# Performance work log

Measured on AMD Instinct MI355X. Metric: run time of the kernel, lower is better.

The kernel has to match this reference:

```python
import jax, jax.numpy as jnp
import numpy as np

B, T, NV, DEG, E = 64, 256, 20000, 8, 128
NSEG, NBUCKET = NV * DEG, 288
F_DIST, F_DIR, F_TT, HID = 50, 50, 50, 100
FEED = 2 * E + F_DIST + F_DIR  # 356


def setup_inputs() -> dict:
    key = jax.random.key(0)
    ks = jax.random.split(key, 32)
    s = 1.0 / np.sqrt(E)
    return {
        "xs_padded": jax.random.randint(ks[0], (B, T), 0, NV),
        "lengths": jax.random.randint(ks[1], (B,), 8, T + 1),
        "xs_actions": jax.random.randint(ks[2], (B, T - 1), 0, DEG),
        "destinations": jax.random.randint(ks[3], (B,), 0, NV),
        "adj_list": jax.random.randint(ks[4], (NV, DEG), 0, NV),
        "seg_ids": jax.random.randint(ks[5], (NV, DEG), 0, NSEG),
        "start_time": 42,
        "locations": jax.random.normal(ks[6], (NV, 2)),
        "time_dist_seg": jax.random.uniform(ks[7], (NSEG, NBUCKET)) * 10.0,
        "emb": jax.random.normal(ks[8], (NV + 2, E)) * 0.01,
        "Wq": jax.random.normal(ks[9], (E, E)) * s,
        "Wk": jax.random.normal(ks[10], (E, E)) * s,
        "Wv": jax.random.normal(ks[11], (E, E)) * s,
        "Wo": jax.random.normal(ks[12], (E, E)) * s,
        "dist_W": jax.random.normal(ks[13], (1, F_DIST)),
        "dist_b": jnp.zeros((F_DIST,)),
        "dir_W": jax.random.normal(ks[14], (2, F_DIR)) * 0.7,
        "dir_b": jnp.zeros((F_DIR,)),
        "tt_W": jax.random.normal(ks[15], (1, F_TT)),
        "tt_b": jnp.zeros((F_TT,)),
        "ob_W1": jax.random.normal(ks[16], (F_TT, F_TT // 2)) * (1.0 / np.sqrt(F_TT)),
        "ob_b1": jnp.zeros((F_TT // 2,)),
        "ob_W2": jax.random.normal(ks[17], (F_TT // 2, 1)) * (1.0 / np.sqrt(F_TT // 2)),
        "ob_b2": jnp.zeros((1,)),
        "om_W1": jax.random.normal(ks[18], (FEED, HID)) * (1.0 / np.sqrt(FEED)),
        "om_b1": jnp.zeros((HID,)),
        "om_W2": jax.random.normal(ks[19], (HID, HID // 2)) * (1.0 / np.sqrt(HID)),
        "om_b2": jnp.zeros((HID // 2,)),
        "om_W3": jax.random.normal(ks[20], (HID // 2, 1)) * (1.0 / np.sqrt(HID // 2)),
        "om_b3": jnp.zeros((1,)),
    }


def reference(xs_padded, lengths, xs_actions, destinations, adj_list, seg_ids,
              start_time, locations, time_dist_seg, emb, Wq, Wk, Wv, Wo,
              dist_W, dist_b, dir_W, dir_b, tt_W, tt_b,
              ob_W1, ob_b1, ob_W2, ob_b2,
              om_W1, om_b1, om_W2, om_b2, om_W3, om_b3):
    # --- embeddings + causal/padding-masked self-attention (flash_att) ---
    x_e = emb[xs_padded]                                       # [B,T,E]
    q, k, v = x_e @ Wq, x_e @ Wk, x_e @ Wv
    scores = jnp.einsum('bqe,bke->bqk', q, k) / jnp.sqrt(jnp.float32(E))
    causal = jnp.triu(jnp.ones((T, T), bool), 1)
    pad = jnp.arange(T)[None, :] >= lengths[:, None]           # key padding [B,T]
    scores = jnp.where(causal[None] | pad[:, None, :], -1e9, scores)
    hidden = jnp.einsum('bqk,bke->bqe', jax.nn.softmax(scores, axis=-1), v) @ Wo

    # --- irregular neighbor gather: route_neighbors only filled for t < len-1 ---
    valid_t = jnp.arange(T)[None, :] < (lengths - 1)[:, None]  # [B,T]
    rn = jnp.where(valid_t[:, :, None], adj_list[xs_padded], 0)  # [B,T,DEG]

    # --- distance to destination feature ---
    dest_c = locations[destinations][:, None, None, :]         # [B,1,1,2]
    nbr_c = locations[rn]                                      # [B,T,DEG,2]
    dist = jnp.abs(nbr_c - dest_c).sum(-1, keepdims=True) * 100.0
    dist_f = dist @ dist_W + dist_b

    # --- direction (unit vector) feature ---
    vec = nbr_c - locations[xs_padded][:, :, None, :]
    unit = vec / (jnp.linalg.norm(vec, axis=-1, keepdims=True) + 1e-8)
    dir_f = unit @ dir_W + dir_b

    # --- travel-time lookup + masked whitening ---
    nmask = rn != 0
    tt = time_dist_seg[seg_ids[xs_padded], start_time]         # [B,T,DEG]
    mf = nmask.astype(tt.dtype)
    cnt = mf.sum()
    mean = (tt * mf).sum() / cnt
    var = (((tt - mean) ** 2) * mf).sum() / (cnt - 1.0)        # unbiased, like torch.std
    tt = (tt - mean) / (jnp.sqrt(var) + 1e-6)
    tt_f = (tt[..., None] @ tt_W + tt_b) * mf[..., None]

    # --- fuse and score neighbors ---
    hid_e = jnp.broadcast_to(hidden[:, :, None, :], (B, T, DEG, E))
    dest_e = jnp.broadcast_to(emb[destinations][:, None, None, :], (B, T, DEG, E))
    feed = jnp.concatenate([hid_e, dist_f, dir_f, dest_e], axis=-1)  # [B,T,DEG,356]

    ob = (jax.nn.relu(tt_f @ ob_W1 + ob_b1) @ ob_W2 + ob_b2).squeeze(-1)
    h1 = jax.nn.relu(feed @ om_W1 + om_b1)
    h2 = jax.nn.relu(h1 @ om_W2 + om_b2)
    logits = (h2 @ om_W3 + om_b3).squeeze(-1) + ob             # [B,T,DEG]

    # --- per-route mean cross-entropy over valid transitions, summed over batch ---
    logp = jax.nn.log_softmax(logits[:, :T - 1], axis=-1)
    nll = -jnp.take_along_axis(logp, xs_actions[..., None], axis=-1).squeeze(-1)
    vmask = (jnp.arange(T - 1)[None, :] < (lengths - 1)[:, None]).astype(nll.dtype)
    per = (nll * vmask).sum(1) / (lengths - 1).astype(nll.dtype)
    return per.sum()
```

## Files before the change

kernel.cpp:

```cpp
#include <hip/hip_runtime.h>
#include <math.h>

#define BB 64
#define TT 256
#define DEG 8
#define EE 128
#define NBUCKET 288
#define HID 100
#define H2 50

constexpr size_t OFF_STATS   = 0;
constexpr size_t OFF_CDIST   = 4;
constexpr size_t OFF_CDIRX   = 104;
constexpr size_t OFF_CDIRY   = 204;
constexpr size_t OFF_BASE    = 304;
constexpr size_t OFF_V25     = 404;
constexpr size_t OFF_C25     = 429;
constexpr size_t OFF_OBZ     = 454;
constexpr size_t OFF_DESTPRE = 456;
constexpr size_t OFF_WF      = 6856;
constexpr size_t OFF_W2P     = 19656;
constexpr size_t OFF_TT      = 32456;
constexpr size_t OFF_Q       = 163528;
constexpr size_t OFF_K       = OFF_Q + 16384 * 128;
constexpr size_t OFF_VP      = OFF_K + 16384 * 128;

__global__ void __launch_bounds__(256) k_setup(
    const int* destinations, const float* emb, const float* Wo,
    const float* dist_W, const float* dist_b, const float* dir_W, const float* dir_b,
    const float* tt_W, const float* tt_b, const float* ob_W1, const float* ob_b1,
    const float* ob_W2, const float* ob_b2, const float* om_W1, const float* om_b1,
    const float* om_W2, float* ws, float* out) {
    __shared__ float sh[EE];
    int blk = blockIdx.x;
    int j = threadIdx.x;
    if (blk == 0) {
        if (j < 4) ws[OFF_STATS + j] = 0.f;
        if (j == 0) out[0] = 0.f;
        if (j < HID) {
            float cd = 0.f, cx = 0.f, cy = 0.f, bs = om_b1[j];
            for (int f = 0; f < 50; f++) {
                float w1d = om_W1[(128 + f) * HID + j];
                float w1r = om_W1[(178 + f) * HID + j];
                cd += dist_W[f] * w1d;
                bs += dist_b[f] * w1d + dir_b[f] * w1r;
                cx += dir_W[f] * w1r;
                cy += dir_W[50 + f] * w1r;
            }
            ws[OFF_CDIST + j] = cd; ws[OFF_CDIRX + j] = cx;
            ws[OFF_CDIRY + j] = cy; ws[OFF_BASE + j] = bs;
        }
        if (j >= 128 && j < 153) {
            int jj = j - 128;
            float v = 0.f, c = ob_b1[jj];
            for (int i = 0; i < 50; i++) {
                v += tt_W[i] * ob_W1[i * 25 + jj];
                c += tt_b[i] * ob_W1[i * 25 + jj];
            }
            ws[OFF_V25 + jj] = v; ws[OFF_C25 + jj] = c;
        }
        if (j == 200) {
            float z = ob_b2[0];
            for (int i = 0; i < 25; i++) z += fmaxf(ob_b1[i], 0.f) * ob_W2[i];
            ws[OFF_OBZ] = z;
        }
    } else if (blk <= 64) {
        int b = blk - 1;
        if (j < EE) sh[j] = emb[(size_t)destinations[b] * EE + j];
        __syncthreads();
        if (j < HID) {
            float acc = 0.f;
            for (int i = 0; i < EE; i++) acc += sh[i] * om_W1[(228 + i) * HID + j];
            ws[OFF_DESTPRE + b * HID + j] = acc;
        }
    } else if (blk <= 192) {
        int i = blk - 65;
        if (j < EE) sh[j] = Wo[i * EE + j];
        __syncthreads();
        if (j < HID) {
            float acc = 0.f;
            for (int jj = 0; jj < EE; jj++) acc += sh[jj] * om_W1[jj * HID + j];
            ws[OFF_WF + i * HID + j] = acc;
        }
    } else {
        for (int idx = j; idx < 5600; idx += 256) {
            int m = idx / 56, n = idx - m * 56;
            ws[OFF_W2P + idx] = (n < H2) ? om_W2[m * H2 + n] : 0.f;
        }
    }
}

__global__ void __launch_bounds__(256) k_mid(
    const int* xs, const int* lengths, const int* adj, const int* seg,
    const int* stime, const float* tds, const float* emb,
    const float* Wq, const float* Wk, const float* Wv, float* ws) {
    __shared__ float smem[2 * 128 * 36 + 32];
    int blk = blockIdx.x;
    int tid = threadIdx.x;
    if (blk < 512) {
        float (*XT)[36]  = (float(*)[36])smem;
        float (*T1T)[36] = (float(*)[36])(smem + 128 * 36);
        int* vids = (int*)(smem + 2 * 128 * 36);
        int r0 = blk * 32;
        if (tid < 32) vids[tid] = xs[r0 + tid];
        __syncthreads();
        for (int c = 0; c < 16; c++) {
            int idx = c * 256 + tid;
            int r = idx >> 7, i = idx & 127;
            XT[i][r] = emb[(size_t)vids[r] * EE + i];
        }
        __syncthreads();
        int cg = tid & 31, rg = tid >> 5;
        const float* Wmats[2] = {Wq, Wk};
        float* Omats[2] = {ws + OFF_Q, ws + OFF_K};
        for (int mtx = 0; mtx < 2; mtx++) {
            const float* W = Wmats[mtx];
            float acc[4][4];
            #pragma unroll
            for (int a = 0; a < 4; a++)
                #pragma unroll
                for (int bb = 0; bb < 4; bb++) acc[a][bb] = 0.f;
            #pragma unroll 4
            for (int i = 0; i < EE; i++) {
                float4 av = *(const float4*)&XT[i][rg << 2];
                float4 wv = *(const float4*)&W[i * EE + (cg << 2)];
                acc[0][0] += av.x * wv.x; acc[0][1] += av.x * wv.y; acc[0][2] += av.x * wv.z; acc[0][3] += av.x * wv.w;
                acc[1][0] += av.y * wv.x; acc[1][1] += av.y * wv.y; acc[1][2] += av.y * wv.z; acc[1][3] += av.y * wv.w;
                acc[2][0] += av.z * wv.x; acc[2][1] += av.z * wv.y; acc[2][2] += av.z * wv.z; acc[2][3] += av.z * wv.w;
                acc[3][0] += av.w * wv.x; acc[3][1] += av.w * wv.y; acc[3][2] += av.w * wv.z; acc[3][3] += av.w * wv.w;
            }
            float* O = Omats[mtx];
            #pragma unroll
            for (int jj = 0; jj < 4; jj++)
                *(float4*)&O[(size_t)(r0 + (rg << 2) + jj) * EE + (cg << 2)] =
                    make_float4(acc[jj][0], acc[jj][1], acc[jj][2], acc[jj][3]);
        }
        {
            float acc[4][4];
            #pragma unroll
            for (int a = 0; a < 4; a++)
                #pragma unroll
                for (int bb = 0; bb < 4; bb++) acc[a][bb] = 0.f;
            #pragma unroll 4
            for (int i = 0; i < EE; i++) {
                float4 av = *(const float4*)&XT[i][rg << 2];
                float4 wv = *(const float4*)&Wv[i * EE + (cg << 2)];
                acc[0][0] += av.x * wv.x; acc[0][1] += av.x * wv.y; acc[0][2] += av.x * wv.z; acc[0][3] += av.x * wv.w;
                acc[1][0] += av.y * wv.x; acc[1][1] += av.y * wv.y; acc[1][2] += av.y * wv.z; acc[1][3] += av.y * wv.w;
                acc[2][0] += av.z * wv.x; acc[2][1] += av.z * wv.y; acc[2][2] += av.z * wv.z; acc[2][3] += av.z * wv.w;
                acc[3][0] += av.w * wv.x; acc[3][1] += av.w * wv.y; acc[3][2] += av.w * wv.z; acc[3][3] += av.w * wv.w;
            }
            #pragma unroll
            for (int jj = 0; jj < 4; jj++)
                #pragma unroll
                for (int ii = 0; ii < 4; ii++)
                    T1T[(cg << 2) + ii][(rg << 2) + jj] = acc[jj][ii];
        }
        __syncthreads();
        if (cg < 25) {
            const float* WF = ws + OFF_WF;
            float acc[4][4];
            #pragma unroll
            for (int a = 0; a < 4; a++)
                #pragma unroll
                for (int bb = 0; bb < 4; bb++) acc[a][bb] = 0.f;
            #pragma unroll 4
            for (int i = 0; i < EE; i++) {
                float4 av = *(const float4*)&T1T[i][rg << 2];
                float4 wv = *(const float4*)&WF[i * HID + (cg << 2)];
                acc[0][0] += av.x * wv.x; acc[0][1] += av.x * wv.y; acc[0][2] += av.x * wv.z; acc[0][3] += av.x * wv.w;
                acc[1][0] += av.y * wv.x; acc[1][1] += av.y * wv.y; acc[1][2] += av.y * wv.z; acc[1][3] += av.y * wv.w;
                acc[2][0] += av.z * wv.x; acc[2][1] += av.z * wv.y; acc[2][2] += av.z * wv.z; acc[2][3] += av.z * wv.w;
                acc[3][0] += av.w * wv.x; acc[3][1] += av.w * wv.y; acc[3][2] += av.w * wv.z; acc[3][3] += av.w * wv.w;
            }
            float* VP = ws + OFF_VP;
            #pragma unroll
            for (int jj = 0; jj < 4; jj++)
                *(float4*)&VP[(size_t)(r0 + (rg << 2) + jj) * HID + (cg << 2)] =
                    make_float4(acc[jj][0], acc[jj][1], acc[jj][2], acc[jj][3]);
        }
    } else {
        float* rs = smem; float* rq = smem + 256; float* rc = smem + 512;
        int st = *stime;
        float lsum = 0.f, lsq = 0.f, lcnt = 0.f;
        int total = BB * TT * DEG;
        for (int idx = (blk - 512) * 256 + tid; idx < total; idx += 256 * 256) {
            int d = idx & 7;
            int bt = idx >> 3;
            int t = bt & 255;
            int b = bt >> 8;
            int len = lengths[b];
            if (t >= len - 1) continue;
            int v = xs[bt];
            int sg = seg[v * DEG + d];
            float tt = tds[(size_t)sg * NBUCKET + st];
            ws[OFF_TT + idx] = tt;
            int a = adj[v * DEG + d];
            if (a != 0) { lsum += tt; lsq += tt * tt; lcnt += 1.f; }
        }
        rs[tid] = lsum; rq[tid] = lsq; rc[tid] = lcnt;
        __syncthreads();
        for (int s = 128; s > 0; s >>= 1) {
            if (tid < s) { rs[tid] += rs[tid + s]; rq[tid] += rq[tid + s]; rc[tid] += rc[tid + s]; }
            __syncthreads();
        }
        if (tid == 0) {
            atomicAdd(&ws[OFF_STATS + 0], rs[0]);
            atomicAdd(&ws[OFF_STATS + 1], rq[0]);
            atomicAdd(&ws[OFF_STATS + 2], rc[0]);
        }
    }
}

__global__ void __launch_bounds__(256, 6) k_attnfinal(
    const int* lengths, const int* xs, const int* xs_actions,
    const int* destinations, const int* adj, const float* locations,
    const float* om_b2, const float* om_W3, const float* om_b3,
    const float* ob_W2, const float* ob_b2,
    float* ws, float* out) {
    int blk = blockIdx.x;
    int tile = 31 - (blk >> 6);
    int b = blk & 63;
    int t0 = tile << 3;
    int len = lengths[b];
    if (t0 >= len - 1) return;
    int nqv = len - 1 - t0; if (nqv > 8) nqv = 8;
    int nk = t0 + 8;
    __shared__ float smem[5264];
    float (*H1P)[100] = (float(*)[100])smem;
    float (*Qs)[132]  = (float(*)[132])(smem + 800);
    float (*S)[260]   = (float(*)[260])(smem + 1856);
    float (*pacc)[8]  = (float(*)[8])(smem + 3936);
    float* CFs   = smem + 800;
    float* distR = smem + 4936;
    float* uxR   = smem + 5000;
    float* uyR   = smem + 5064;
    float* obR   = smem + 5128;
    float* lgS   = smem + 5192;
    float* nllS  = smem + 5256;
    int tid = threadIdx.x;
    if (tid < 8) nllS[tid] = 0.f;
    {
        const float* Qg = ws + OFF_Q + (size_t)(b * TT + t0) * EE;
        int r = tid >> 5, c4 = (tid & 31) << 2;
        *(float4*)&Qs[r][c4] = *(const float4*)&Qg[r * EE + c4];
    }
    __syncthreads();
    {
        const float* Kg = ws + OFF_K + (size_t)(b * TT) * EE;
        int w = tid >> 6;
        int key = (tid >> 2) & 15, chunk = tid & 3;
        int coff = chunk << 5;
        for (int k0 = w << 4; k0 < nk; k0 += 64) {
            int kk = k0 + key;
            if (kk < nk) {
                float4 kf[8];
                const float4* Kr = (const float4*)&Kg[(size_t)kk * EE + coff];
                #pragma unroll
                for (int j = 0; j < 8; j++) kf[j] = Kr[j];
                #pragma unroll
                for (int q = 0; q < 8; q++) {
                    const float4* qr = (const float4*)&Qs[q][coff];
                    float s = 0.f;
                    #pragma unroll
                    for (int j = 0; j < 8; j++) {
                        float4 a = qr[j], x = kf[j];
                        s += a.x * x.x + a.y * x.y + a.z * x.z + a.w * x.w;
                    }
                    s += __shfl_xor(s, 1, 64);
                    s += __shfl_xor(s, 2, 64);
                    if (chunk == 0) S[q][kk] = s * 0.08838834764831845f;
                }
            }
        }
    }
    __syncthreads();
    if (tid < 128) {
        int q = tid >> 4, li = tid & 15;
        int tq = t0 + q;
        float sreg[16];
        float mx = -1e30f;
        #pragma unroll
        for (int m = 0; m < 16; m++) {
            int k = li + (m << 4);
            float sv = (k < nk && k <= tq) ? S[q][k] : -1e30f;
            sreg[m] = sv;
            mx = fmaxf(mx, sv);
        }
        #pragma unroll
        for (int o = 1; o < 16; o <<= 1) mx = fmaxf(mx, __shfl_xor(mx, o, 16));
        float ls = 0.f;
        #pragma unroll
        for (int m = 0; m < 16; m++) {
            float p = __expf(sreg[m] - mx);
            sreg[m] = p; ls += p;
        }
        #pragma unroll
        for (int o = 1; o < 16; o <<= 1) ls += __shfl_xor(ls, o, 16);
        float inv = 1.f / ls;
        #pragma unroll
        for (int m = 0; m < 16; m++) S[q][li + (m << 4)] = sreg[m] * inv;
    } else if (tid < 192) {
        const float* CD = ws + OFF_CDIST;
        const float* CX = ws + OFF_CDIRX;
        const float* CY = ws + OFF_CDIRY;
        for (int idx = tid - 128; idx < 400; idx += 64) {
            int m = idx >> 2, c = idx & 3;
            float v = 0.f;
            if (c == 0) v = CD[m];
            else if (c == 1) v = CX[m];
            else if (c == 2) v = CY[m];
            CFs[idx] = v;
        }
    } else {
        int fid = tid - 192;
        int ql = fid >> 3, d = fid & 7;
        int t = t0 + ql;
        int bt = b * TT + t;
        int v = xs[bt];
        int a = adj[v * DEG + d];
        float nbx = locations[2 * a], nby = locations[2 * a + 1];
        int dst = destinations[b];
        float dxl = locations[2 * dst], dyl = locations[2 * dst + 1];
        float cxl = locations[2 * v], cyl = locations[2 * v + 1];
        distR[fid] = (fabsf(nbx - dxl) + fabsf(nby - dyl)) * 100.f;
        float vx = nbx - cxl, vy = nby - cyl;
        float nrm = sqrtf(vx * vx + vy * vy) + 1e-8f;
        uxR[fid] = vx / nrm; uyR[fid] = vy / nrm;
        float sum = ws[OFF_STATS], sq = ws[OFF_STATS + 1], cnt = ws[OFF_STATS + 2];
        float smean = sum / cnt;
        float var = (sq - cnt * smean * smean) / (cnt - 1.f);
        float sdinv = 1.f / (sqrtf(var) + 1e-6f);
        float ttn = (ws[OFF_TT + (size_t)bt * 8 + d] - smean) * sdinv;
        float obp = 0.f;
        for (int j = 0; j < 25; j++)
            obp += fmaxf(ttn * ws[OFF_V25 + j] + ws[OFF_C25 + j], 0.f) * ob_W2[j];
        obR[fid] = (a != 0) ? (obp + ob_b2[0]) : ws[OFF_OBZ];
    }
    __syncthreads();
    {
        int kc = tid >> 7;
        int q = (tid >> 4) & 7, cg = tid & 15;
        float acc[8];
        #pragma unroll
        for (int j = 0; j < 8; j++) acc[j] = 0.f;
        if (cg < 13) {
            const float* VPg = ws + OFF_VP + (size_t)(b * TT) * HID;
            int o0 = cg << 3;
            int o1 = o0 + 4; if (o1 > 96) o1 = 96;
            #pragma unroll 2
            for (int k = kc; k < nk; k += 2) {
                float p = S[q][k];
                const float* vr = &VPg[(size_t)k * HID];
                float4 v0 = *(const float4*)&vr[o0];
                float4 v1 = *(const float4*)&vr[o1];
                acc[0] += p * v0.x; acc[1] += p * v0.y;
                acc[2] += p * v0.z; acc[3] += p * v0.w;
                acc[4] += p * v1.x; acc[5] += p * v1.y;
                acc[6] += p * v1.z; acc[7] += p * v1.w;
            }
        }
        if (kc == 1 && cg < 13) {
            float* pp = &pacc[(q << 4) + cg][0];
            *(float4*)&pp[0] = make_float4(acc[0], acc[1], acc[2], acc[3]);
            *(float4*)&pp[4] = make_float4(acc[4], acc[5], acc[6], acc[7]);
        }
        __syncthreads();
        if (kc == 0 && cg < 13) {
            const float* pp = &pacc[(q << 4) + cg][0];
            const float* BASEv = ws + OFF_BASE;
            const float* DP = ws + OFF_DESTPRE + b * HID;
            int c0 = cg << 3;
            #pragma unroll
            for (int j = 0; j < 8; j++) {
                int c = c0 + j;
                if (c < HID) H1P[q][c] = acc[j] + pp[j] + BASEv[c] + DP[c];
            }
        }
    }
    __syncthreads();
    {
        int lane = tid & 63, w = tid >> 6;
        int rg = (w << 2) | (lane >> 4);
        int half = (lane >> 3) & 1;
        int cg = lane & 7;
        int r0 = rg << 2, n0 = cg << 3;
        const float* Hq = &smem[(rg >> 1) * 100];
        float4 dv4 = *(const float4*)&distR[r0];
        float4 ux4 = *(const float4*)&uxR[r0];
        float4 uy4 = *(const float4*)&uyR[r0];
        float facc[4][8];
        #pragma unroll
        for (int jr = 0; jr < 4; jr++)
            #pragma unroll
            for (int k = 0; k < 8; k++) facc[jr][k] = 0.f;
        if (cg < 7) {
            const float* W2P = ws + OFF_W2P;
            int m0 = half * 50;
            #pragma unroll 2
            for (int mi = 0; mi < 50; mi++) {
                int m = m0 + mi;
                float4 cf = *(const float4*)&CFs[m << 2];
                float hq = Hq[m];
                float h0 = fmaxf(hq + dv4.x * cf.x + ux4.x * cf.y + uy4.x * cf.z, 0.f);
                float h1 = fmaxf(hq + dv4.y * cf.x + ux4.y * cf.y + uy4.y * cf.z, 0.f);
                float h2 = fmaxf(hq + dv4.z * cf.x + ux4.z * cf.y + uy4.z * cf.z, 0.f);
                float h3 = fmaxf(hq + dv4.w * cf.x + ux4.w * cf.y + uy4.w * cf.z, 0.f);
                const float* wrow = &W2P[m * 56 + n0];
                float4 w0 = *(const float4*)&wrow[0];
                float4 w1 = *(const float4*)&wrow[4];
                facc[0][0] += h0 * w0.x; facc[0][1] += h0 * w0.y; facc[0][2] += h0 * w0.z; facc[0][3] += h0 * w0.w;
                facc[0][4] += h0 * w1.x; facc[0][5] += h0 * w1.y; facc[0][6] += h0 * w1.z; facc[0][7] += h0 * w1.w;
                facc[1][0] += h1 * w0.x; facc[1][1] += h1 * w0.y; facc[1][2] += h1 * w0.z; facc[1][3] += h1 * w0.w;
                facc[1][4] += h1 * w1.x; facc[1][5] += h1 * w1.y; facc[1][6] += h1 * w1.z; facc[1][7] += h1 * w1.w;
                facc[2][0] += h2 * w0.x; facc[2][1] += h2 * w0.y; facc[2][2] += h2 * w0.z; facc[2][3] += h2 * w0.w;
                facc[2][4] += h2 * w1.x; facc[2][5] += h2 * w1.y; facc[2][6] += h2 * w1.z; facc[2][7] += h2 * w1.w;
                facc[3][0] += h3 * w0.x; facc[3][1] += h3 * w0.y; facc[3][2] += h3 * w0.z; facc[3][3] += h3 * w0.w;
                facc[3][4] += h3 * w1.x; facc[3][5] += h3 * w1.y; facc[3][6] += h3 * w1.z; facc[3][7] += h3 * w1.w;
            }
        }
        #pragma unroll
        for (int jr = 0; jr < 4; jr++)
            #pragma unroll
            for (int k = 0; k < 8; k++)
                facc[jr][k] += __shfl_xor(facc[jr][k], 8, 64);
        float parts[4] = {0.f, 0.f, 0.f, 0.f};
        if (cg < 7) {
            float b2v[8], w3v[8];
            #pragma unroll
            for (int k = 0; k < 8; k++) {
                int n = n0 + k;
                b2v[k] = (n < H2) ? om_b2[n] : 0.f;
                w3v[k] = (n < H2) ? om_W3[n] : 0.f;
            }
            #pragma unroll
            for (int jr = 0; jr < 4; jr++) {
                float part = 0.f;
                #pragma unroll
                for (int k = 0; k < 8; k++)
                    part += fmaxf(facc[jr][k] + b2v[k], 0.f) * w3v[k];
                parts[jr] = part;
            }
        }
        float ob3 = om_b3[0];
        #pragma unroll
        for (int jr = 0; jr < 4; jr++) {
            float part = parts[jr];
            part += __shfl_xor(part, 1, 64);
            part += __shfl_xor(part, 2, 64);
            part += __shfl_xor(part, 4, 64);
            if ((lane & 15) == 0) lgS[r0 + jr] = part + ob3 + obR[r0 + jr];
        }
    }
    __syncthreads();
    if (tid < 8) {
        int qa = tid;
        if (qa < nqv) {
            float lg[8];
            float mxl = -1e30f;
            #pragma unroll
            for (int d = 0; d < 8; d++) {
                lg[d] = lgS[(qa << 3) + d];
                mxl = fmaxf(mxl, lg[d]);
            }
            int act = xs_actions[b * (TT - 1) + t0 + qa];
            float se = 0.f, sel = 0.f;
            #pragma unroll
            for (int d = 0; d < 8; d++) {
                se += __expf(lg[d] - mxl);
                if (d == act) sel = lg[d];
            }
            float nll = mxl + __logf(se) - sel;
            nllS[qa] = nll / (float)(len - 1);
        }
    }
    __syncthreads();
    if (tid == 0) {
        float s = 0.f;
        #pragma unroll
        for (int i = 0; i < 8; i++) s += nllS[i];
        atomicAdd(out, s);
    }
}

extern "C" void kernel_launch(void* const* d_in, const int* in_sizes, int n_in,
                              void* d_out, int out_size, void* d_ws, size_t ws_size,
                              hipStream_t stream) {
    const int* xs_padded    = (const int*)d_in[0];
    const int* lengths      = (const int*)d_in[1];
    const int* xs_actions   = (const int*)d_in[2];
    const int* destinations = (const int*)d_in[3];
    const int* adj_list     = (const int*)d_in[4];
    const int* seg_ids      = (const int*)d_in[5];
    const int* start_time   = (const int*)d_in[6];
    const float* locations  = (const float*)d_in[7];
    const float* tds        = (const float*)d_in[8];
    const float* emb        = (const float*)d_in[9];
    const float* Wq         = (const float*)d_in[10];
    const float* Wk         = (const float*)d_in[11];
    const float* Wv         = (const float*)d_in[12];
    const float* Wo         = (const float*)d_in[13];
    const float* dist_W     = (const float*)d_in[14];
    const float* dist_b     = (const float*)d_in[15];
    const float* dir_W      = (const float*)d_in[16];
    const float* dir_b      = (const float*)d_in[17];
    const float* tt_W       = (const float*)d_in[18];
    const float* tt_b       = (const float*)d_in[19];
    const float* ob_W1      = (const float*)d_in[20];
    const float* ob_b1      = (const float*)d_in[21];
    const float* ob_W2      = (const float*)d_in[22];
    const float* ob_b2      = (const float*)d_in[23];
    const float* om_W1      = (const float*)d_in[24];
    const float* om_b1      = (const float*)d_in[25];
    const float* om_W2      = (const float*)d_in[26];
    const float* om_b2      = (const float*)d_in[27];
    const float* om_W3      = (const float*)d_in[28];
    const float* om_b3      = (const float*)d_in[29];
    float* ws  = (float*)d_ws;
    float* out = (float*)d_out;

    k_setup<<<194, 256, 0, stream>>>(destinations, emb, Wo, dist_W, dist_b,
                                     dir_W, dir_b, tt_W, tt_b, ob_W1, ob_b1,
                                     ob_W2, ob_b2, om_W1, om_b1, om_W2, ws, out);
    k_mid<<<768, 256, 0, stream>>>(xs_padded, lengths, adj_list, seg_ids,
                                   start_time, tds, emb, Wq, Wk, Wv, ws);
    k_attnfinal<<<BB * 32, 256, 0, stream>>>(
        lengths, xs_padded, xs_actions, destinations, adj_list, locations,
        om_b2, om_W3, om_b3, ob_W2, ob_b2, ws, out);
}
```

Measured before the change: 459.3 us.

## Double k_attnfinal block size to 512 threads and split work finer

Launches the attention/final kernel with 512 threads per block instead of 256. The QK score loop strides over more waves, the P·V accumulation is split four ways with three partial sums reduced through shared memory, and the MLP stage gives each thread 2 rows instead of 4. The goal is more parallelism per block and shorter per-thread serial chains on the latency-bound per-(batch, tile) work. The cost is more shared memory, more syncs covering idle threads, and possibly fewer resident blocks under the launch bounds.

```diff
diff --git a/kernel.cpp b/kernel.cpp
--- a/kernel.cpp
+++ b/kernel.cpp
@@ -212,7 +212,7 @@
     }
 }
 
-__global__ void __launch_bounds__(256, 6) k_attnfinal(
+__global__ void __launch_bounds__(512, 6) k_attnfinal(
     const int* lengths, const int* xs, const int* xs_actions,
     const int* destinations, const int* adj, const float* locations,
     const float* om_b2, const float* om_W3, const float* om_b3,
@@ -226,21 +226,21 @@
     if (t0 >= len - 1) return;
     int nqv = len - 1 - t0; if (nqv > 8) nqv = 8;
     int nk = t0 + 8;
-    __shared__ float smem[5264];
+    __shared__ float smem[7336];
     float (*H1P)[100] = (float(*)[100])smem;
     float (*Qs)[132]  = (float(*)[132])(smem + 800);
     float (*S)[260]   = (float(*)[260])(smem + 1856);
     float (*pacc)[8]  = (float(*)[8])(smem + 3936);
     float* CFs   = smem + 800;
-    float* distR = smem + 4936;
-    float* uxR   = smem + 5000;
-    float* uyR   = smem + 5064;
-    float* obR   = smem + 5128;
-    float* lgS   = smem + 5192;
-    float* nllS  = smem + 5256;
+    float* distR = smem + 7008;
+    float* uxR   = smem + 7072;
+    float* uyR   = smem + 7136;
+    float* obR   = smem + 7200;
+    float* lgS   = smem + 7264;
+    float* nllS  = smem + 7328;
     int tid = threadIdx.x;
     if (tid < 8) nllS[tid] = 0.f;
-    {
+    if (tid < 256) {
         const float* Qg = ws + OFF_Q + (size_t)(b * TT + t0) * EE;
         int r = tid >> 5, c4 = (tid & 31) << 2;
         *(float4*)&Qs[r][c4] = *(const float4*)&Qg[r * EE + c4];
@@ -251,7 +251,7 @@
         int w = tid >> 6;
         int key = (tid >> 2) & 15, chunk = tid & 3;
         int coff = chunk << 5;
-        for (int k0 = w << 4; k0 < nk; k0 += 64) {
+        for (int k0 = w << 4; k0 < nk; k0 += 128) {
             int kk = k0 + key;
             if (kk < nk) {
                 float4 kf[8];
@@ -312,7 +312,7 @@
             else if (c == 2) v = CY[m];
             CFs[idx] = v;
         }
-    } else {
+    } else if (tid < 256) {
         int fid = tid - 192;
         int ql = fid >> 3, d = fid & 7;
         int t = t0 + ql;
@@ -348,8 +348,8 @@
             const float* VPg = ws + OFF_VP + (size_t)(b * TT) * HID;
             int o0 = cg << 3;
             int o1 = o0 + 4; if (o1 > 96) o1 = 96;
-            #pragma unroll 2
-            for (int k = kc; k < nk; k += 2) {
+            #pragma unroll 4
+            for (int k = kc; k < nk; k += 4) {
                 float p = S[q][k];
                 const float* vr = &VPg[(size_t)k * HID];
                 float4 v0 = *(const float4*)&vr[o0];
@@ -360,38 +360,40 @@
                 acc[6] += p * v1.z; acc[7] += p * v1.w;
             }
         }
-        if (kc == 1 && cg < 13) {
-            float* pp = &pacc[(q << 4) + cg][0];
+        if (kc > 0 && cg < 13) {
+            float* pp = &pacc[((kc - 1) << 7) + (q << 4) + cg][0];
             *(float4*)&pp[0] = make_float4(acc[0], acc[1], acc[2], acc[3]);
             *(float4*)&pp[4] = make_float4(acc[4], acc[5], acc[6], acc[7]);
         }
         __syncthreads();
         if (kc == 0 && cg < 13) {
-            const float* pp = &pacc[(q << 4) + cg][0];
+            const float* p1 = &pacc[(q << 4) + cg][0];
+            const float* p2 = &pacc[128 + (q << 4) + cg][0];
+            const float* p3 = &pacc[256 + (q << 4) + cg][0];
             const float* BASEv = ws + OFF_BASE;
             const float* DP = ws + OFF_DESTPRE + b * HID;
             int c0 = cg << 3;
             #pragma unroll
             for (int j = 0; j < 8; j++) {
                 int c = c0 + j;
-                if (c < HID) H1P[q][c] = acc[j] + pp[j] + BASEv[c] + DP[c];
+                if (c < HID) H1P[q][c] = acc[j] + p1[j] + p2[j] + p3[j] + BASEv[c] + DP[c];
             }
         }
     }
     __syncthreads();
     {
-        int lane = tid & 63, w = tid >> 6;
-        int rg = (w << 2) | (lane >> 4);
+        int lane = tid & 63, w8 = tid >> 6;
+        int rg = (w8 << 2) | (lane >> 4);
         int half = (lane >> 3) & 1;
         int cg = lane & 7;
-        int r0 = rg << 2, n0 = cg << 3;
-        const float* Hq = &smem[(rg >> 1) * 100];
-        float4 dv4 = *(const float4*)&distR[r0];
-        float4 ux4 = *(const float4*)&uxR[r0];
-        float4 uy4 = *(const float4*)&uyR[r0];
-        float facc[4][8];
-        #pragma unroll
-        for (int jr = 0; jr < 4; jr++)
+        int r0 = rg << 1, n0 = cg << 3;
+        const float* Hq = &smem[(rg >> 2) * 100];
+        float2 dv2 = *(const float2*)&distR[r0];
+        float2 ux2 = *(const float2*)&uxR[r0];
+        float2 uy2 = *(const float2*)&uyR[r0];
+        float facc[2][8];
+        #pragma unroll
+        for (int jr = 0; jr < 2; jr++)
             #pragma unroll
             for (int k = 0; k < 8; k++) facc[jr][k] = 0.f;
         if (cg < 7) {
@@ -402,10 +404,8 @@
                 int m = m0 + mi;
                 float4 cf = *(const float4*)&CFs[m << 2];
                 float hq = Hq[m];
-                float h0 = fmaxf(hq + dv4.x * cf.x + ux4.x * cf.y + uy4.x * cf.z, 0.f);
-                float h1 = fmaxf(hq + dv4.y * cf.x + ux4.y * cf.y + uy4.y * cf.z, 0.f);
-                float h2 = fmaxf(hq + dv4.z * cf.x + ux4.z * cf.y + uy4.z * cf.z, 0.f);
-                float h3 = fmaxf(hq + dv4.w * cf.x + ux4.w * cf.y + uy4.w * cf.z, 0.f);
+                float h0 = fmaxf(hq + dv2.x * cf.x + ux2.x * cf.y + uy2.x * cf.z, 0.f);
+                float h1 = fmaxf(hq + dv2.y * cf.x + ux2.y * cf.y + uy2.y * cf.z, 0.f);
                 const float* wrow = &W2P[m * 56 + n0];
                 float4 w0 = *(const float4*)&wrow[0];
                 float4 w1 = *(const float4*)&wrow[4];
@@ -413,18 +413,14 @@
                 facc[0][4] += h0 * w1.x; facc[0][5] += h0 * w1.y; facc[0][6] += h0 * w1.z; facc[0][7] += h0 * w1.w;
                 facc[1][0] += h1 * w0.x; facc[1][1] += h1 * w0.y; facc[1][2] += h1 * w0.z; facc[1][3] += h1 * w0.w;
                 facc[1][4] += h1 * w1.x; facc[1][5] += h1 * w1.y; facc[1][6] += h1 * w1.z; facc[1][7] += h1 * w1.w;
-                facc[2][0] += h2 * w0.x; facc[2][1] += h2 * w0.y; facc[2][2] += h2 * w0.z; facc[2][3] += h2 * w0.w;
-                facc[2][4] += h2 * w1.x; facc[2][5] += h2 * w1.y; facc[2][6] += h2 * w1.z; facc[2][7] += h2 * w1.w;
-                facc[3][0] += h3 * w0.x; facc[3][1] += h3 * w0.y; facc[3][2] += h3 * w0.z; facc[3][3] += h3 * w0.w;
-                facc[3][4] += h3 * w1.x; facc[3][5] += h3 * w1.y; facc[3][6] += h3 * w1.z; facc[3][7] += h3 * w1.w;
-            }
-        }
-        #pragma unroll
-        for (int jr = 0; jr < 4; jr++)
+            }
+        }
+        #pragma unroll
+        for (int jr = 0; jr < 2; jr++)
             #pragma unroll
             for (int k = 0; k < 8; k++)
                 facc[jr][k] += __shfl_xor(facc[jr][k], 8, 64);
-        float parts[4] = {0.f, 0.f, 0.f, 0.f};
+        float parts[2] = {0.f, 0.f};
         if (cg < 7) {
             float b2v[8], w3v[8];
             #pragma unroll
@@ -434,7 +430,7 @@
                 w3v[k] = (n < H2) ? om_W3[n] : 0.f;
             }
             #pragma unroll
-            for (int jr = 0; jr < 4; jr++) {
+            for (int jr = 0; jr < 2; jr++) {
                 float part = 0.f;
                 #pragma unroll
                 for (int k = 0; k < 8; k++)
@@ -444,7 +440,7 @@
         }
         float ob3 = om_b3[0];
         #pragma unroll
-        for (int jr = 0; jr < 4; jr++) {
+        for (int jr = 0; jr < 2; jr++) {
             float part = parts[jr];
             part += __shfl_xor(part, 1, 64);
             part += __shfl_xor(part, 2, 64);
@@ -524,7 +520,7 @@
                                      ob_W2, ob_b2, om_W1, om_b1, om_W2, ws, out);
     k_mid<<<768, 256, 0, stream>>>(xs_padded, lengths, adj_list, seg_ids,
                                    start_time, tds, emb, Wq, Wk, Wv, ws);
-    k_attnfinal<<<BB * 32, 256, 0, stream>>>(
+    k_attnfinal<<<BB * 32, 512, 0, stream>>>(
         lengths, xs_padded, xs_actions, destinations, adj_list, locations,
         om_b2, om_W3, om_b3, ob_W2, ob_b2, ws, out);
 }
```

Result: no change. 457.7 us (-0.3%).

## Split attention-final kernel into attention and MLP-scoring kernels via workspace slots

Applied to the files above, without the earlier changes.

The fused attention+scoring kernel is split into two launches. k_attnA runs with 512 threads, doubling the key-loop and P·V split-k parallelism, and writes H1 pre-activations plus the per-neighbor features to a per-block workspace slot. k_attnB reloads that slot and runs the MLP and cross-entropy with a smaller shared-memory footprint. The aim is more parallelism per block in the attention phase and better occupancy in each phase. The cost is an extra kernel launch and a global round-trip of about 1 KB per block.

```diff
diff --git a/kernel.cpp b/kernel.cpp
--- a/kernel.cpp
+++ b/kernel.cpp
@@ -24,6 +24,7 @@
 constexpr size_t OFF_Q       = 163528;
 constexpr size_t OFF_K       = OFF_Q + 16384 * 128;
 constexpr size_t OFF_VP      = OFF_K + 16384 * 128;
+constexpr size_t OFF_H1S     = 6000000;
 
 __global__ void __launch_bounds__(256) k_setup(
     const int* destinations, const float* emb, const float* Wo,
@@ -212,35 +213,24 @@
     }
 }
 
-__global__ void __launch_bounds__(256, 6) k_attnfinal(
-    const int* lengths, const int* xs, const int* xs_actions,
-    const int* destinations, const int* adj, const float* locations,
-    const float* om_b2, const float* om_W3, const float* om_b3,
-    const float* ob_W2, const float* ob_b2,
-    float* ws, float* out) {
+__global__ void __launch_bounds__(512) k_attnA(
+    const int* lengths, const int* xs, const int* destinations, const int* adj,
+    const float* locations, const float* ob_W2, const float* ob_b2,
+    float* ws) {
     int blk = blockIdx.x;
     int tile = 31 - (blk >> 6);
     int b = blk & 63;
     int t0 = tile << 3;
     int len = lengths[b];
     if (t0 >= len - 1) return;
-    int nqv = len - 1 - t0; if (nqv > 8) nqv = 8;
     int nk = t0 + 8;
-    __shared__ float smem[5264];
-    float (*H1P)[100] = (float(*)[100])smem;
-    float (*Qs)[132]  = (float(*)[132])(smem + 800);
-    float (*S)[260]   = (float(*)[260])(smem + 1856);
-    float (*pacc)[8]  = (float(*)[8])(smem + 3936);
-    float* CFs   = smem + 800;
-    float* distR = smem + 4936;
-    float* uxR   = smem + 5000;
-    float* uyR   = smem + 5064;
-    float* obR   = smem + 5128;
-    float* lgS   = smem + 5192;
-    float* nllS  = smem + 5256;
+    __shared__ float smem[6208];
+    float (*Qs)[132]  = (float(*)[132])smem;
+    float (*S)[260]   = (float(*)[260])(smem + 1056);
+    float (*pacc)[8]  = (float(*)[8])(smem + 3136);
+    float* slot = ws + OFF_H1S + (size_t)blk * 1088;
     int tid = threadIdx.x;
-    if (tid < 8) nllS[tid] = 0.f;
-    {
+    if (tid < 256) {
         const float* Qg = ws + OFF_Q + (size_t)(b * TT + t0) * EE;
         int r = tid >> 5, c4 = (tid & 31) << 2;
         *(float4*)&Qs[r][c4] = *(const float4*)&Qg[r * EE + c4];
@@ -251,7 +241,7 @@
         int w = tid >> 6;
         int key = (tid >> 2) & 15, chunk = tid & 3;
         int coff = chunk << 5;
-        for (int k0 = w << 4; k0 < nk; k0 += 64) {
+        for (int k0 = w << 4; k0 < nk; k0 += 128) {
             int kk = k0 + key;
             if (kk < nk) {
                 float4 kf[8];
@@ -300,19 +290,7 @@
         float inv = 1.f / ls;
         #pragma unroll
         for (int m = 0; m < 16; m++) S[q][li + (m << 4)] = sreg[m] * inv;
-    } else if (tid < 192) {
-        const float* CD = ws + OFF_CDIST;
-        const float* CX = ws + OFF_CDIRX;
-        const float* CY = ws + OFF_CDIRY;
-        for (int idx = tid - 128; idx < 400; idx += 64) {
-            int m = idx >> 2, c = idx & 3;
-            float v = 0.f;
-            if (c == 0) v = CD[m];
-            else if (c == 1) v = CX[m];
-            else if (c == 2) v = CY[m];
-            CFs[idx] = v;
-        }
-    } else {
+    } else if (tid >= 192 && tid < 256) {
         int fid = tid - 192;
         int ql = fid >> 3, d = fid & 7;
         int t = t0 + ql;
@@ -323,10 +301,11 @@
         int dst = destinations[b];
         float dxl = locations[2 * dst], dyl = locations[2 * dst + 1];
         float cxl = locations[2 * v], cyl = locations[2 * v + 1];
-        distR[fid] = (fabsf(nbx - dxl) + fabsf(nby - dyl)) * 100.f;
+        slot[800 + fid] = (fabsf(nbx - dxl) + fabsf(nby - dyl)) * 100.f;
         float vx = nbx - cxl, vy = nby - cyl;
         float nrm = sqrtf(vx * vx + vy * vy) + 1e-8f;
-        uxR[fid] = vx / nrm; uyR[fid] = vy / nrm;
+        slot[864 + fid] = vx / nrm;
+        slot[928 + fid] = vy / nrm;
         float sum = ws[OFF_STATS], sq = ws[OFF_STATS + 1], cnt = ws[OFF_STATS + 2];
         float smean = sum / cnt;
         float var = (sq - cnt * smean * smean) / (cnt - 1.f);
@@ -335,7 +314,7 @@
         float obp = 0.f;
         for (int j = 0; j < 25; j++)
             obp += fmaxf(ttn * ws[OFF_V25 + j] + ws[OFF_C25 + j], 0.f) * ob_W2[j];
-        obR[fid] = (a != 0) ? (obp + ob_b2[0]) : ws[OFF_OBZ];
+        slot[992 + fid] = (a != 0) ? (obp + ob_b2[0]) : ws[OFF_OBZ];
     }
     __syncthreads();
     {
@@ -348,8 +327,8 @@
             const float* VPg = ws + OFF_VP + (size_t)(b * TT) * HID;
             int o0 = cg << 3;
             int o1 = o0 + 4; if (o1 > 96) o1 = 96;
-            #pragma unroll 2
-            for (int k = kc; k < nk; k += 2) {
+            #pragma unroll 4
+            for (int k = kc; k < nk; k += 4) {
                 float p = S[q][k];
                 const float* vr = &VPg[(size_t)k * HID];
                 float4 v0 = *(const float4*)&vr[o0];
@@ -360,22 +339,55 @@
                 acc[6] += p * v1.z; acc[7] += p * v1.w;
             }
         }
-        if (kc == 1 && cg < 13) {
-            float* pp = &pacc[(q << 4) + cg][0];
+        if (kc > 0 && cg < 13) {
+            float* pp = &pacc[((kc - 1) << 7) + (q << 4) + cg][0];
             *(float4*)&pp[0] = make_float4(acc[0], acc[1], acc[2], acc[3]);
             *(float4*)&pp[4] = make_float4(acc[4], acc[5], acc[6], acc[7]);
         }
         __syncthreads();
         if (kc == 0 && cg < 13) {
-            const float* pp = &pacc[(q << 4) + cg][0];
+            const float* p1 = &pacc[(q << 4) + cg][0];
+            const float* p2 = &pacc[128 + (q << 4) + cg][0];
+            const float* p3 = &pacc[256 + (q << 4) + cg][0];
             const float* BASEv = ws + OFF_BASE;
             const float* DP = ws + OFF_DESTPRE + b * HID;
             int c0 = cg << 3;
             #pragma unroll
             for (int j = 0; j < 8; j++) {
                 int c = c0 + j;
-                if (c < HID) H1P[q][c] = acc[j] + pp[j] + BASEv[c] + DP[c];
-            }
+                if (c < HID) slot[q * HID + c] = acc[j] + p1[j] + p2[j] + p3[j] + BASEv[c] + DP[c];
+            }
+        }
+    }
+}
+
+__global__ void __launch_bounds__(256) k_attnB(
+    const int* lengths, const int* xs_actions,
+    const float* om_b2, const float* om_W3, const float* om_b3,
+    float* ws, float* out) {
+    int blk = blockIdx.x;
+    int tile = 31 - (blk >> 6);
+    int b = blk & 63;
+    int t0 = tile << 3;
+    int len = lengths[b];
+    if (t0 >= len - 1) return;
+    int nqv = len - 1 - t0; if (nqv > 8) nqv = 8;
+    __shared__ float smem[1528];
+    const float* slot = ws + OFF_H1S + (size_t)blk * 1088;
+    int tid = threadIdx.x;
+    if (tid < 8) smem[1520 + tid] = 0.f;
+    for (int i = tid; i < 1056; i += 256) smem[i] = slot[i];
+    {
+        const float* CD = ws + OFF_CDIST;
+        const float* CX = ws + OFF_CDIRX;
+        const float* CY = ws + OFF_CDIRY;
+        for (int i = tid; i < 400; i += 256) {
+            int m = i >> 2, c = i & 3;
+            float v = 0.f;
+            if (c == 0) v = CD[m];
+            else if (c == 1) v = CX[m];
+            else if (c == 2) v = CY[m];
+            smem[1056 + i] = v;
         }
     }
     __syncthreads();
@@ -385,10 +397,10 @@
         int half = (lane >> 3) & 1;
         int cg = lane & 7;
         int r0 = rg << 2, n0 = cg << 3;
-        const float* Hq = &smem[(rg >> 1) * 100];
-        float4 dv4 = *(const float4*)&distR[r0];
-        float4 ux4 = *(const float4*)&uxR[r0];
-        float4 uy4 = *(const float4*)&uyR[r0];
+        const float* Hq = &smem[(rg >> 1) * HID];
+        float4 dv4 = *(const float4*)&smem[800 + r0];
+        float4 ux4 = *(const float4*)&smem[864 + r0];
+        float4 uy4 = *(const float4*)&smem[928 + r0];
         float facc[4][8];
         #pragma unroll
         for (int jr = 0; jr < 4; jr++)
@@ -396,6 +408,7 @@
             for (int k = 0; k < 8; k++) facc[jr][k] = 0.f;
         if (cg < 7) {
             const float* W2P = ws + OFF_W2P;
+            const float* CFs = smem + 1056;
             int m0 = half * 50;
             #pragma unroll 2
             for (int mi = 0; mi < 50; mi++) {
@@ -449,7 +462,7 @@
             part += __shfl_xor(part, 1, 64);
             part += __shfl_xor(part, 2, 64);
             part += __shfl_xor(part, 4, 64);
-            if ((lane & 15) == 0) lgS[r0 + jr] = part + ob3 + obR[r0 + jr];
+            if ((lane & 15) == 0) smem[1456 + r0 + jr] = part + ob3 + smem[992 + r0 + jr];
         }
     }
     __syncthreads();
@@ -460,7 +473,7 @@
             float mxl = -1e30f;
             #pragma unroll
             for (int d = 0; d < 8; d++) {
-                lg[d] = lgS[(qa << 3) + d];
+                lg[d] = smem[1456 + (qa << 3) + d];
                 mxl = fmaxf(mxl, lg[d]);
             }
             int act = xs_actions[b * (TT - 1) + t0 + qa];
@@ -471,14 +484,14 @@
                 if (d == act) sel = lg[d];
             }
             float nll = mxl + __logf(se) - sel;
-            nllS[qa] = nll / (float)(len - 1);
+            smem[1520 + qa] = nll / (float)(len - 1);
         }
     }
     __syncthreads();
     if (tid == 0) {
         float s = 0.f;
         #pragma unroll
-        for (int i = 0; i < 8; i++) s += nllS[i];
+        for (int i = 0; i < 8; i++) s += smem[1520 + i];
         atomicAdd(out, s);
     }
 }
@@ -524,7 +537,8 @@
                                      ob_W2, ob_b2, om_W1, om_b1, om_W2, ws, out);
     k_mid<<<768, 256, 0, stream>>>(xs_padded, lengths, adj_list, seg_ids,
                                    start_time, tds, emb, Wq, Wk, Wv, ws);
-    k_attnfinal<<<BB * 32, 256, 0, stream>>>(
-        lengths, xs_padded, xs_actions, destinations, adj_list, locations,
-        om_b2, om_W3, om_b3, ob_W2, ob_b2, ws, out);
+    k_attnA<<<BB * 32, 512, 0, stream>>>(
+        lengths, xs_padded, destinations, adj_list, locations, ob_W2, ob_b2, ws);
+    k_attnB<<<BB * 32, 256, 0, stream>>>(
+        lengths, xs_actions, om_b2, om_W3, om_b3, ws, out);
 }
```

After: 455.0 us. Within noise of the previous version (-0.9%).
